# Optimization experiments

Measured on AMD Instinct MI355X. Metric: run time of the kernel, lower is better.

## Reference

```python
import jax, jax.numpy as jnp
import numpy as np

IN_F = 1024
OUT_F = 4096
SEARCH_SPACE = [1, 2, 4, 8, 16]  # block sizes; powers of 2 dividing both dims, capped at 16


def circ_avg(W, bs):
    """Project W [out,in] onto block-circulant structure with block size bs.

    Equivalent to trans_to_cir_meng: within each (bs x bs) block, average each
    wrap-around diagonal and rebuild a circulant block C[k, j] = c[(k - j) % bs].
    """
    q, p = W.shape[0] // bs, W.shape[1] // bs
    t = W.reshape(q, bs, p, bs).transpose(0, 2, 1, 3)  # [q, p, bs, bs]
    i = jnp.arange(bs)
    # rot[..., i, j] = t[..., i, (i + j) % bs]  (rotate rows so diagonals align in columns)
    rot = t[:, :, i[:, None], (i[:, None] + i[None, :]) % bs]  # [q, p, bs, bs]
    c = rot.mean(axis=2)  # [q, p, bs]  mean over each diagonal
    # circulant block: w[..., k, j] = c[..., (k - j) % bs]
    w = c[:, :, (i[:, None] - i[None, :]) % bs]  # [q, p, bs, bs]
    return w.transpose(0, 2, 1, 3).reshape(W.shape)


def setup_inputs() -> dict:
    key = jax.random.key(0)
    k1, k2, k3, k4 = jax.random.split(key, 4)
    x = jax.random.normal(k1, (16, 512, IN_F), dtype=jnp.float32)
    weight = jax.random.normal(k2, (OUT_F, IN_F), dtype=jnp.float32) * 0.02
    alphas = jax.random.normal(k3, (len(SEARCH_SPACE),), dtype=jnp.float32)
    bias = jax.random.normal(k4, (OUT_F,), dtype=jnp.float32) * 0.02
    return {"x": x, "weight": weight, "alphas": alphas, "bias": bias}


def reference(x, weight, alphas, bias):
    # soft NAS mixture over block sizes (tau=1, soft mode)
    a = jax.nn.softmax(alphas)
    W = a[0] * weight  # block_size 1 == original weight
    for idx, bs in enumerate(SEARCH_SPACE[1:], start=1):
        W = W + a[idx] * circ_avg(weight, bs)
    # F.linear: y = x @ W^T + b
    return jnp.einsum("bsi,oi->bso", x, W) + bias
```

## Files before the change

### kernel.cpp

```cpp
#include <hip/hip_runtime.h>

typedef __bf16 bf16;
typedef __bf16 bf16x8 __attribute__((ext_vector_type(8)));
typedef float floatx4 __attribute__((ext_vector_type(4)));

#define IN_F  1024
#define OUT_F 4096
#define M_DIM 8192
#define K_DIM 1024
#define N_DIM 4096

__device__ __forceinline__ unsigned short f2bf(float f) {
    unsigned int u = __float_as_uint(f);
    u += 0x7FFFu + ((u >> 16) & 1u);
    return (unsigned short)(u >> 16);
}

__global__ __launch_bounds__(256) void build_w_kernel(
    const float* __restrict__ W, const float* __restrict__ alphas,
    unsigned short* __restrict__ Wb)
{
    __shared__ __align__(16) float Wl[16 * 256];
    __shared__ __align__(16) float D2[2048];
    __shared__ float D4[1024];
    __shared__ float D8[512];
    __shared__ float D16[256];

    const int t = threadIdx.x;
    const int rb = blockIdx.x >> 2;
    const int cb = blockIdx.x & 3;
    const int row0 = rb * 16, col0 = cb * 256;

    const float4* src = (const float4*)(W + (size_t)row0 * IN_F + col0);
    #pragma unroll
    for (int j = 0; j < 4; ++j) {
        const int idx = j * 256 + t;
        const int r = idx >> 6, c4 = idx & 63;
        ((float4*)Wl)[r * 64 + c4] = src[(size_t)r * 256 + c4];
    }

    float av[5];
    float mx = -1e30f;
    #pragma unroll
    for (int j = 0; j < 5; ++j) { av[j] = alphas[j]; mx = fmaxf(mx, av[j]); }
    float s = 0.f;
    #pragma unroll
    for (int j = 0; j < 5; ++j) { av[j] = __expf(av[j] - mx); s += av[j]; }
    const float inv = 1.f / s;
    #pragma unroll
    for (int j = 0; j < 5; ++j) av[j] *= inv;
    #pragma unroll
    for (int e = 1; e <= 4; ++e) av[e] *= 1.0f / (float)(1 << e);

    __syncthreads();

    {
        const int c16 = t >> 4, d = t & 15;
        float acc = 0.f;
        #pragma unroll
        for (int r = 0; r < 16; ++r)
            acc += Wl[r * 256 + c16 * 16 + ((r + d) & 15)];
        D16[t] = acc;
    }
    #pragma unroll
    for (int it = 0; it < 2; ++it) {
        const int s8 = t + it * 256;
        const int d = s8 & 7, c8 = (s8 >> 3) & 31, r8 = s8 >> 8;
        float acc = 0.f;
        #pragma unroll
        for (int r = 0; r < 8; ++r)
            acc += Wl[(r8 * 8 + r) * 256 + c8 * 8 + ((r + d) & 7)];
        D8[s8] = acc;
    }
    #pragma unroll
    for (int it = 0; it < 4; ++it) {
        const int s4 = t + it * 256;
        const int d = s4 & 3, c4 = (s4 >> 2) & 63, r4 = s4 >> 8;
        float acc = 0.f;
        #pragma unroll
        for (int r = 0; r < 4; ++r)
            acc += Wl[(r4 * 4 + r) * 256 + c4 * 4 + ((r + d) & 3)];
        D4[s4] = acc;
    }
    #pragma unroll
    for (int it = 0; it < 8; ++it) {
        const int s2 = t + it * 256;
        const int d = s2 & 1, c2 = (s2 >> 1) & 127, r2 = s2 >> 8;
        D2[s2] = Wl[(r2 * 2) * 256 + c2 * 2 + d]
               + Wl[(r2 * 2 + 1) * 256 + c2 * 2 + ((1 + d) & 1)];
    }

    __syncthreads();

    const int k = t >> 4, jj = t & 15;
    float res[16];
    #pragma unroll
    for (int jb = 0; jb < 16; ++jb) {
        const int col = jb * 16 + jj;
        const int dd = k - col;
        res[jb] = av[0] * Wl[k * 256 + col]
                + av[1] * D2[((k >> 1) * 128 + (col >> 1)) * 2 + (dd & 1)]
                + av[2] * D4[((k >> 2) * 64  + (col >> 2)) * 4 + (dd & 3)]
                + av[3] * D8[((k >> 3) * 32  + (col >> 3)) * 8 + (dd & 7)]
                + av[4] * D16[(col >> 4) * 16 + (dd & 15)];
    }

    __syncthreads();
    unsigned short* st = (unsigned short*)D2;
    #pragma unroll
    for (int jb = 0; jb < 16; ++jb)
        st[k * 256 + jb * 16 + jj] = f2bf(res[jb]);
    __syncthreads();

    const uint4* p = (const uint4*)(st + k * 256 + jj * 16);
    uint4* dst = (uint4*)(Wb + (size_t)(row0 + k) * IN_F + col0 + jj * 16);
    dst[0] = p[0];
    dst[1] = p[1];
}

__global__ __launch_bounds__(256) void cvt_x_kernel(
    const float* __restrict__ x, uint4* __restrict__ xb)
{
    const int t = blockIdx.x * 256 + threadIdx.x;
    const float4* xv = (const float4*)x;
    const float4 v0 = xv[2 * t];
    const float4 v1 = xv[2 * t + 1];
    uint4 o;
    o.x = (unsigned)f2bf(v0.x) | ((unsigned)f2bf(v0.y) << 16);
    o.y = (unsigned)f2bf(v0.z) | ((unsigned)f2bf(v0.w) << 16);
    o.z = (unsigned)f2bf(v1.x) | ((unsigned)f2bf(v1.y) << 16);
    o.w = (unsigned)f2bf(v1.z) | ((unsigned)f2bf(v1.w) << 16);
    xb[t] = o;
}

__global__ __launch_bounds__(256) void gemm_bt_kernel(
    const bf16* __restrict__ A, const bf16* __restrict__ B,
    const float* __restrict__ bias, float* __restrict__ C)
{
    constexpr int N = N_DIM, K = K_DIM;
    constexpr int TM = 128, TN = 128, TK = 64;
    constexpr int NBLK = (M_DIM / TM) * (N_DIM / TN);

    __shared__ __align__(16) bf16 As[TM * TK];
    __shared__ __align__(16) bf16 Bs[TN * TK];

    const int t    = threadIdx.x;
    const int w    = t >> 6;
    const int l    = t & 63;
    const int quad = l >> 4;
    const int l16  = l & 15;
    const int x7   = l16 & 7;

    const int nb = N / TN;
    const int wgid = (blockIdx.x & 7) * (NBLK >> 3) + (blockIdx.x >> 3);
    const int bm = wgid / nb;
    const int bn = wgid % nb;

    const int wm = (w >> 1) * 64;
    const int wn = (w & 1) * 64;

    floatx4 acc[4][4] = {};

    int crow[4], ccol[4], loff[4];
    #pragma unroll
    for (int q = 0; q < 4; ++q) {
        const int chunk = q * 256 + t;
        crow[q] = chunk >> 3;
        ccol[q] = (((chunk & 7) ^ ((chunk >> 3) & 7)) * 8);
        loff[q] = (q * 256 + (t & ~63)) * 8;
    }

    const bf16* Abase = A + (size_t)bm * TM * K;
    const bf16* Bbase = B + (size_t)bn * TN * K;

    for (int kt = 0; kt < K; kt += TK) {
        #pragma unroll
        for (int q = 0; q < 4; ++q) {
            __builtin_amdgcn_global_load_lds(
                (const __attribute__((address_space(1))) void*)(Abase + (size_t)crow[q] * K + kt + ccol[q]),
                (__attribute__((address_space(3))) void*)(As + loff[q]), 16, 0, 0);
        }
        #pragma unroll
        for (int q = 0; q < 4; ++q) {
            __builtin_amdgcn_global_load_lds(
                (const __attribute__((address_space(1))) void*)(Bbase + (size_t)crow[q] * K + kt + ccol[q]),
                (__attribute__((address_space(3))) void*)(Bs + loff[q]), 16, 0, 0);
        }
        __syncthreads();

        #pragma unroll
        for (int ks = 0; ks < 2; ++ks) {
            bf16x8 af[4], bfr[4];
            const int kx = ((ks * 4 + quad) ^ x7) * 8;
            #pragma unroll
            for (int mt = 0; mt < 4; ++mt)
                af[mt] = *(const bf16x8*)(As + (wm + mt * 16 + l16) * TK + kx);
            #pragma unroll
            for (int nt = 0; nt < 4; ++nt)
                bfr[nt] = *(const bf16x8*)(Bs + (wn + nt * 16 + l16) * TK + kx);
            #pragma unroll
            for (int mt = 0; mt < 4; ++mt)
                #pragma unroll
                for (int nt = 0; nt < 4; ++nt)
                    acc[mt][nt] = __builtin_amdgcn_mfma_f32_16x16x32_bf16(
                        af[mt], bfr[nt], acc[mt][nt], 0, 0, 0);
        }
        __syncthreads();
    }

    float bv[4];
    #pragma unroll
    for (int nt = 0; nt < 4; ++nt)
        bv[nt] = bias[bn * TN + wn + nt * 16 + l16];

    float* Cbase = C + (size_t)(bm * TM + wm) * N + bn * TN + wn;
    #pragma unroll
    for (int mt = 0; mt < 4; ++mt) {
        #pragma unroll
        for (int r = 0; r < 4; ++r) {
            float* crowp = Cbase + (size_t)(mt * 16 + quad * 4 + r) * N;
            #pragma unroll
            for (int nt = 0; nt < 4; ++nt)
                crowp[nt * 16 + l16] = acc[mt][nt][r] + bv[nt];
        }
    }
}

extern "C" void kernel_launch(void* const* d_in, const int* in_sizes, int n_in,
                              void* d_out, int out_size, void* d_ws, size_t ws_size,
                              hipStream_t stream) {
    const float* x      = (const float*)d_in[0];
    const float* weight = (const float*)d_in[1];
    const float* alphas = (const float*)d_in[2];
    const float* bias   = (const float*)d_in[3];
    float* out = (float*)d_out;

    unsigned short* Wb = (unsigned short*)d_ws;
    unsigned short* Xb = (unsigned short*)((char*)d_ws + (size_t)OUT_F * IN_F * 2);

    build_w_kernel<<<(OUT_F / 16) * (IN_F / 256), 256, 0, stream>>>(weight, alphas, Wb);
    cvt_x_kernel<<<(M_DIM * K_DIM / 8) / 256, 256, 0, stream>>>(x, (uint4*)Xb);

    const int grid = (M_DIM / 128) * (N_DIM / 128);
    gemm_bt_kernel<<<grid, 256, 0, stream>>>((const bf16*)Xb, (const bf16*)Wb, bias, out);
}
```

Baseline: 248.4 us.

## Triple-buffer GEMM LDS staging with 256x128 tiles and 512-thread blocks

Result: faster. 237.6 us (-4.4%).

```diff
diff --git a/kernel.cpp b/kernel.cpp
--- a/kernel.cpp
+++ b/kernel.cpp
@@ -133,16 +133,21 @@
     xb[t] = o;
 }
 
-__global__ __launch_bounds__(256) void gemm_bt_kernel(
+#define TM 256
+#define TN 128
+#define TK 64
+#define A_SLOT_EL (TM * TK)
+#define B_SLOT_EL (TN * TK)
+#define SLOT_EL   (A_SLOT_EL + B_SLOT_EL)
+
+__global__ __launch_bounds__(512, 2) void gemm_bt_kernel(
     const bf16* __restrict__ A, const bf16* __restrict__ B,
     const float* __restrict__ bias, float* __restrict__ C)
 {
     constexpr int N = N_DIM, K = K_DIM;
-    constexpr int TM = 128, TN = 128, TK = 64;
-    constexpr int NBLK = (M_DIM / TM) * (N_DIM / TN);
-
-    __shared__ __align__(16) bf16 As[TM * TK];
-    __shared__ __align__(16) bf16 Bs[TN * TK];
+    constexpr int NT = K / TK;
+
+    __shared__ __align__(16) bf16 smem[3 * SLOT_EL];
 
     const int t    = threadIdx.x;
     const int w    = t >> 6;
@@ -152,9 +157,8 @@
     const int x7   = l16 & 7;
 
     const int nb = N / TN;
-    const int wgid = (blockIdx.x & 7) * (NBLK >> 3) + (blockIdx.x >> 3);
-    const int bm = wgid / nb;
-    const int bn = wgid % nb;
+    const int bm = blockIdx.x / nb;
+    const int bn = blockIdx.x % nb;
 
     const int wm = (w >> 1) * 64;
     const int wn = (w & 1) * 64;
@@ -164,49 +168,86 @@
     int crow[4], ccol[4], loff[4];
     #pragma unroll
     for (int q = 0; q < 4; ++q) {
-        const int chunk = q * 256 + t;
+        const int chunk = q * 512 + t;
         crow[q] = chunk >> 3;
-        ccol[q] = (((chunk & 7) ^ ((chunk >> 3) & 7)) * 8);
-        loff[q] = (q * 256 + (t & ~63)) * 8;
+        ccol[q] = ((chunk & 7) ^ ((chunk >> 3) & 7)) * 8;
+        loff[q] = (q * 512 + (t & ~63)) * 8;
     }
 
     const bf16* Abase = A + (size_t)bm * TM * K;
     const bf16* Bbase = B + (size_t)bn * TN * K;
 
-    for (int kt = 0; kt < K; kt += TK) {
-        #pragma unroll
-        for (int q = 0; q < 4; ++q) {
-            __builtin_amdgcn_global_load_lds(
-                (const __attribute__((address_space(1))) void*)(Abase + (size_t)crow[q] * K + kt + ccol[q]),
-                (__attribute__((address_space(3))) void*)(As + loff[q]), 16, 0, 0);
-        }
-        #pragma unroll
-        for (int q = 0; q < 4; ++q) {
-            __builtin_amdgcn_global_load_lds(
-                (const __attribute__((address_space(1))) void*)(Bbase + (size_t)crow[q] * K + kt + ccol[q]),
-                (__attribute__((address_space(3))) void*)(Bs + loff[q]), 16, 0, 0);
-        }
-        __syncthreads();
-
-        #pragma unroll
-        for (int ks = 0; ks < 2; ++ks) {
-            bf16x8 af[4], bfr[4];
-            const int kx = ((ks * 4 + quad) ^ x7) * 8;
-            #pragma unroll
-            for (int mt = 0; mt < 4; ++mt)
-                af[mt] = *(const bf16x8*)(As + (wm + mt * 16 + l16) * TK + kx);
-            #pragma unroll
-            for (int nt = 0; nt < 4; ++nt)
-                bfr[nt] = *(const bf16x8*)(Bs + (wn + nt * 16 + l16) * TK + kx);
-            #pragma unroll
-            for (int mt = 0; mt < 4; ++mt)
-                #pragma unroll
-                for (int nt = 0; nt < 4; ++nt)
-                    acc[mt][nt] = __builtin_amdgcn_mfma_f32_16x16x32_bf16(
-                        af[mt], bfr[nt], acc[mt][nt], 0, 0, 0);
-        }
-        __syncthreads();
-    }
+#define STAGE_A(KT, SLOT)                                                        \
+    do {                                                                         \
+        _Pragma("unroll")                                                        \
+        for (int q = 0; q < 4; ++q)                                              \
+            __builtin_amdgcn_global_load_lds(                                    \
+                (const __attribute__((address_space(1))) void*)(                 \
+                    Abase + (size_t)crow[q] * K + (KT) * TK + ccol[q]),          \
+                (__attribute__((address_space(3))) void*)((SLOT) + loff[q]),     \
+                16, 0, 0);                                                       \
+    } while (0)
+
+#define STAGE_B(KT, SLOT)                                                        \
+    do {                                                                         \
+        _Pragma("unroll")                                                        \
+        for (int q = 0; q < 2; ++q)                                              \
+            __builtin_amdgcn_global_load_lds(                                    \
+                (const __attribute__((address_space(1))) void*)(                 \
+                    Bbase + (size_t)crow[q] * K + (KT) * TK + ccol[q]),          \
+                (__attribute__((address_space(3))) void*)((SLOT) + A_SLOT_EL +   \
+                                                          loff[q]),              \
+                16, 0, 0);                                                       \
+    } while (0)
+
+#define PHASE(SA, SB, KS, STAGE_STMT)                                            \
+    do {                                                                         \
+        bf16x8 af[4], bfr[4];                                                    \
+        const int kx = (((KS) * 4 + quad) ^ x7) * 8;                             \
+        _Pragma("unroll")                                                        \
+        for (int mt = 0; mt < 4; ++mt)                                           \
+            af[mt] = *(const bf16x8*)((SA) + (wm + mt * 16 + l16) * TK + kx);    \
+        _Pragma("unroll")                                                        \
+        for (int nt = 0; nt < 4; ++nt)                                           \
+            bfr[nt] = *(const bf16x8*)((SB) + (wn + nt * 16 + l16) * TK + kx);   \
+        STAGE_STMT;                                                              \
+        __builtin_amdgcn_s_barrier();                                            \
+        __builtin_amdgcn_s_setprio(1);                                           \
+        _Pragma("unroll")                                                        \
+        for (int mt = 0; mt < 4; ++mt)                                           \
+            _Pragma("unroll")                                                    \
+            for (int nt = 0; nt < 4; ++nt)                                       \
+                acc[mt][nt] = __builtin_amdgcn_mfma_f32_16x16x32_bf16(           \
+                    af[mt], bfr[nt], acc[mt][nt], 0, 0, 0);                      \
+        __builtin_amdgcn_s_setprio(0);                                           \
+    } while (0)
+
+    bf16* s0 = smem;
+    bf16* s1 = smem + SLOT_EL;
+    bf16* s2 = smem + 2 * SLOT_EL;
+    STAGE_A(0, s0); STAGE_B(0, s0);
+    STAGE_A(1, s1); STAGE_B(1, s1);
+
+    #pragma unroll 1
+    for (int kt = 0; kt < NT; ++kt) {
+        if (kt == NT - 1)
+            asm volatile("s_waitcnt vmcnt(0)" ::: "memory");
+        else
+            asm volatile("s_waitcnt vmcnt(6)" ::: "memory");
+        __builtin_amdgcn_s_barrier();
+
+        bf16* Sa = s0;
+        bf16* Sb = s0 + A_SLOT_EL;
+        const bool st = (kt + 2 < NT);
+
+        PHASE(Sa, Sb, 0, if (st) STAGE_A(kt + 2, s2));
+        PHASE(Sa, Sb, 1, if (st) STAGE_B(kt + 2, s2));
+
+        bf16* tmp = s0; s0 = s1; s1 = s2; s2 = tmp;
+    }
+#undef PHASE
+#undef STAGE_A
+#undef STAGE_B
 
     float bv[4];
     #pragma unroll
@@ -241,6 +282,6 @@
     build_w_kernel<<<(OUT_F / 16) * (IN_F / 256), 256, 0, stream>>>(weight, alphas, Wb);
     cvt_x_kernel<<<(M_DIM * K_DIM / 8) / 256, 256, 0, stream>>>(x, (uint4*)Xb);
 
-    const int grid = (M_DIM / 128) * (N_DIM / 128);
-    gemm_bt_kernel<<<grid, 256, 0, stream>>>((const bf16*)Xb, (const bf16*)Wb, bias, out);
-}
+    const int grid = (M_DIM / TM) * (N_DIM / TN);
+    gemm_bt_kernel<<<grid, 512, 0, stream>>>((const bf16*)Xb, (const bf16*)Wb, bias, out);
+}
```

## Rewrite GEMM with 256x256 tiles and a 9-slot multi-stage async LDS pipeline

Applied to the files above, without the earlier changes.

Measured after the change: 233.2 us. -6.1%, faster.

```diff
diff --git a/kernel.cpp b/kernel.cpp
--- a/kernel.cpp
+++ b/kernel.cpp
@@ -133,95 +133,178 @@
     xb[t] = o;
 }
 
-__global__ __launch_bounds__(256) void gemm_bt_kernel(
+#define TM 256
+#define TN 256
+#define TK 64
+#define HALF_EL 8192
+#define NSLOT 9
+
+__global__ __launch_bounds__(512, 2) void gemm_bt_kernel(
     const bf16* __restrict__ A, const bf16* __restrict__ B,
     const float* __restrict__ bias, float* __restrict__ C)
 {
     constexpr int N = N_DIM, K = K_DIM;
-    constexpr int TM = 128, TN = 128, TK = 64;
-    constexpr int NBLK = (M_DIM / TM) * (N_DIM / TN);
-
-    __shared__ __align__(16) bf16 As[TM * TK];
-    __shared__ __align__(16) bf16 Bs[TN * TK];
+
+    __shared__ __align__(16) bf16 smem[NSLOT * HALF_EL];
 
     const int t    = threadIdx.x;
     const int w    = t >> 6;
     const int l    = t & 63;
     const int quad = l >> 4;
     const int l16  = l & 15;
-    const int x7   = l16 & 7;
+
+    const int wr = w >> 2;
+    const int wc = w & 3;
+    const int wm = wr * 128;
+    const int wn = wc * 64;
 
     const int nb = N / TN;
-    const int wgid = (blockIdx.x & 7) * (NBLK >> 3) + (blockIdx.x >> 3);
-    const int bm = wgid / nb;
-    const int bn = wgid % nb;
-
-    const int wm = (w >> 1) * 64;
-    const int wn = (w & 1) * 64;
-
-    floatx4 acc[4][4] = {};
-
-    int crow[4], ccol[4], loff[4];
-    #pragma unroll
-    for (int q = 0; q < 4; ++q) {
-        const int chunk = q * 256 + t;
-        crow[q] = chunk >> 3;
-        ccol[q] = (((chunk & 7) ^ ((chunk >> 3) & 7)) * 8);
-        loff[q] = (q * 256 + (t & ~63)) * 8;
-    }
-
-    const bf16* Abase = A + (size_t)bm * TM * K;
-    const bf16* Bbase = B + (size_t)bn * TN * K;
-
-    for (int kt = 0; kt < K; kt += TK) {
+    const int bm = blockIdx.x / nb;
+    const int bn = blockIdx.x % nb;
+
+    const int fko = l16 * 32 + ((quad ^ ((l16 >> 1) & 3)) * 8);
+
+    int sloff0, sloff1;
+    const bf16 *As0p, *As1p, *Bs0p, *Bs1p;
+    {
+        const int c0 = t, c1 = 512 + t;
+        const int r0 = c0 >> 2, r1 = c1 >> 2;
+        const int k0 = ((c0 & 3) ^ ((c0 >> 3) & 3)) * 8;
+        const int k1 = ((c1 & 3) ^ ((c1 >> 3) & 3)) * 8;
+        sloff0 = (t & ~63) * 8;
+        sloff1 = (512 + (t & ~63)) * 8;
+        const bf16* Abase = A + (size_t)bm * TM * K;
+        const bf16* Bbase = B + (size_t)bn * TN * K;
+        As0p = Abase + (size_t)r0 * K + k0;
+        As1p = Abase + (size_t)r1 * K + k1;
+        Bs0p = Bbase + (size_t)r0 * K + k0;
+        Bs1p = Bbase + (size_t)r1 * K + k1;
+    }
+
+    floatx4 acc[8][4] = {};
+
+#define GLL(SRC, DST)                                                         \
+    __builtin_amdgcn_global_load_lds(                                         \
+        (const __attribute__((address_space(1))) void*)(SRC),                 \
+        (__attribute__((address_space(3))) void*)(DST), 16, 0, 0)
+
+#define STAGE(TT, J, SL) do {                                                 \
+        const bf16* g0_ = ((J) & 1) ? Bs0p : As0p;                            \
+        const bf16* g1_ = ((J) & 1) ? Bs1p : As1p;                            \
+        const int ko_ = (TT) * TK + ((J) >> 1) * 32;                          \
+        bf16* lb_ = smem + (SL) * HALF_EL;                                    \
+        GLL(g0_ + ko_, lb_ + sloff0);                                         \
+        GLL(g1_ + ko_, lb_ + sloff1);                                         \
+    } while (0)
+
+#define MF(d, va, vb)                                                         \
+    d = __builtin_amdgcn_mfma_f32_16x16x32_bf16(va, vb, d, 0, 0, 0)
+
+    STAGE(0, 0, 0); STAGE(0, 1, 1); STAGE(0, 2, 2); STAGE(0, 3, 3);
+    STAGE(1, 0, 4); STAGE(1, 1, 5); STAGE(1, 2, 6);
+
+    bf16x8 af[8], bfr[4];
+    int s4 = 0;
+
+#define TILE_BODY(T, V0, V2, DO0, DO1, DO2, DO3) do {                         \
+    const int slA0 = s4;                                                      \
+    const int slB0 = s4 + 1 - ((s4 + 1 >= NSLOT) ? NSLOT : 0);                \
+    const int slA1 = s4 + 2 - ((s4 + 2 >= NSLOT) ? NSLOT : 0);                \
+    const int slB1 = s4 + 3 - ((s4 + 3 >= NSLOT) ? NSLOT : 0);                \
+    const int sp0  = s4 + 7 - ((s4 + 7 >= NSLOT) ? NSLOT : 0);                \
+    const int sp1  = s4 + 8 - ((s4 + 8 >= NSLOT) ? NSLOT : 0);                \
+                               \
+    asm volatile("s_waitcnt vmcnt(" V0 ")" ::: "memory");                     \
+    __builtin_amdgcn_s_barrier();                                             \
+    {                                                                         \
+        const bf16* a0_ = smem + slA0 * HALF_EL + wm * 32 + fko;              \
+        const bf16* b0_ = smem + slB0 * HALF_EL + wn * 32 + fko;              \
+        _Pragma("unroll")                                                     \
+        for (int m = 0; m < 8; ++m)                                           \
+            af[m] = *(const bf16x8*)(a0_ + m * 512);                          \
+        bfr[0] = *(const bf16x8*)(b0_);                                       \
+        bfr[1] = *(const bf16x8*)(b0_ + 512);                                 \
+        if (DO0) STAGE((T) + 1, 3, sp0);                                      \
+        __builtin_amdgcn_s_setprio(1);                                        \
+        _Pragma("unroll")                                                     \
+        for (int m = 0; m < 8; ++m) {                                         \
+            MF(acc[m][0], af[m], bfr[0]);                                     \
+            MF(acc[m][1], af[m], bfr[1]);                                     \
+        }                                                                     \
+        __builtin_amdgcn_s_setprio(0);                                        \
+                                     \
+        __builtin_amdgcn_s_barrier();                                         \
+        bfr[2] = *(const bf16x8*)(b0_ + 1024);                                \
+        bfr[3] = *(const bf16x8*)(b0_ + 1536);                                \
+        if (DO1) STAGE((T) + 2, 0, sp1);                                      \
+        __builtin_amdgcn_s_setprio(1);                                        \
+        _Pragma("unroll")                                                     \
+        for (int m = 0; m < 8; ++m) {                                         \
+            MF(acc[m][2], af[m], bfr[2]);                                     \
+            MF(acc[m][3], af[m], bfr[3]);                                     \
+        }                                                                     \
+        __builtin_amdgcn_s_setprio(0);                                        \
+    }                                                                         \
+                             \
+    asm volatile("s_waitcnt vmcnt(" V2 ")" ::: "memory");                     \
+    __builtin_amdgcn_s_barrier();                                             \
+    {                                                                         \
+        const bf16* a1_ = smem + slA1 * HALF_EL + wm * 32 + fko;              \
+        const bf16* b1_ = smem + slB1 * HALF_EL + wn * 32 + fko;              \
+        _Pragma("unroll")                                                     \
+        for (int m = 0; m < 8; ++m)                                           \
+            af[m] = *(const bf16x8*)(a1_ + m * 512);                          \
+        bfr[0] = *(const bf16x8*)(b1_);                                       \
+        bfr[1] = *(const bf16x8*)(b1_ + 512);                                 \
+        if (DO2) STAGE((T) + 2, 1, slA0);      \
+        __builtin_amdgcn_s_setprio(1);                                        \
+        _Pragma("unroll")                                                     \
+        for (int m = 0; m < 8; ++m) {                                         \
+            MF(acc[m][0], af[m], bfr[0]);                                     \
+            MF(acc[m][1], af[m], bfr[1]);                                     \
+        }                                                                     \
+        __builtin_amdgcn_s_setprio(0);                                        \
+                                                \
+        __builtin_amdgcn_s_barrier();                                         \
+        bfr[2] = *(const bf16x8*)(b1_ + 1024);                                \
+        bfr[3] = *(const bf16x8*)(b1_ + 1536);                                \
+        if (DO3) STAGE((T) + 2, 2, slB0);      \
+        __builtin_amdgcn_s_setprio(1);                                        \
+        _Pragma("unroll")                                                     \
+        for (int m = 0; m < 8; ++m) {                                         \
+            MF(acc[m][2], af[m], bfr[2]);                                     \
+            MF(acc[m][3], af[m], bfr[3]);                                     \
+        }                                                                     \
+        __builtin_amdgcn_s_setprio(0);                                        \
+    }                                                                         \
+    s4 += 4; if (s4 >= NSLOT) s4 -= NSLOT;                                    \
+} while (0)
+
+    #pragma unroll 1
+    for (int T = 0; T < 14; ++T)
+        TILE_BODY(T, "10", "10", true, true, true, true);
+    TILE_BODY(14, "10", "8", true, false, false, false);
+    TILE_BODY(15, "4",  "0", false, false, false, false);
+
+#undef TILE_BODY
+#undef STAGE
+#undef GLL
+#undef MF
+
+    float bv[4];
+    #pragma unroll
+    for (int nt = 0; nt < 4; ++nt)
+        bv[nt] = bias[bn * TN + wn + nt * 16 + l16];
+
+    float* Cbase = C + (size_t)(bm * TM + wm) * N + bn * TN + wn;
+    #pragma unroll
+    for (int m = 0; m < 8; ++m) {
         #pragma unroll
-        for (int q = 0; q < 4; ++q) {
-            __builtin_amdgcn_global_load_lds(
-                (const __attribute__((address_space(1))) void*)(Abase + (size_t)crow[q] * K + kt + ccol[q]),
-                (__attribute__((address_space(3))) void*)(As + loff[q]), 16, 0, 0);
-        }
-        #pragma unroll
-        for (int q = 0; q < 4; ++q) {
-            __builtin_amdgcn_global_load_lds(
-                (const __attribute__((address_space(1))) void*)(Bbase + (size_t)crow[q] * K + kt + ccol[q]),
-                (__attribute__((address_space(3))) void*)(Bs + loff[q]), 16, 0, 0);
-        }
-        __syncthreads();
-
-        #pragma unroll
-        for (int ks = 0; ks < 2; ++ks) {
-            bf16x8 af[4], bfr[4];
-            const int kx = ((ks * 4 + quad) ^ x7) * 8;
-            #pragma unroll
-            for (int mt = 0; mt < 4; ++mt)
-                af[mt] = *(const bf16x8*)(As + (wm + mt * 16 + l16) * TK + kx);
+        for (int r = 0; r < 4; ++r) {
+            float* crowp = Cbase + (size_t)(m * 16 + quad * 4 + r) * N;
             #pragma unroll
             for (int nt = 0; nt < 4; ++nt)
-                bfr[nt] = *(const bf16x8*)(Bs + (wn + nt * 16 + l16) * TK + kx);
-            #pragma unroll
-            for (int mt = 0; mt < 4; ++mt)
-                #pragma unroll
-                for (int nt = 0; nt < 4; ++nt)
-                    acc[mt][nt] = __builtin_amdgcn_mfma_f32_16x16x32_bf16(
-                        af[mt], bfr[nt], acc[mt][nt], 0, 0, 0);
-        }
-        __syncthreads();
-    }
-
-    float bv[4];
-    #pragma unroll
-    for (int nt = 0; nt < 4; ++nt)
-        bv[nt] = bias[bn * TN + wn + nt * 16 + l16];
-
-    float* Cbase = C + (size_t)(bm * TM + wm) * N + bn * TN + wn;
-    #pragma unroll
-    for (int mt = 0; mt < 4; ++mt) {
-        #pragma unroll
-        for (int r = 0; r < 4; ++r) {
-            float* crowp = Cbase + (size_t)(mt * 16 + quad * 4 + r) * N;
-            #pragma unroll
-            for (int nt = 0; nt < 4; ++nt)
-                crowp[nt * 16 + l16] = acc[mt][nt][r] + bv[nt];
+                crowp[nt * 16 + l16] = acc[m][nt][r] + bv[nt];
         }
     }
 }
@@ -241,6 +324,6 @@
     build_w_kernel<<<(OUT_F / 16) * (IN_F / 256), 256, 0, stream>>>(weight, alphas, Wb);
     cvt_x_kernel<<<(M_DIM * K_DIM / 8) / 256, 256, 0, stream>>>(x, (uint4*)Xb);
 
-    const int grid = (M_DIM / 128) * (N_DIM / 128);
-    gemm_bt_kernel<<<grid, 256, 0, stream>>>((const bf16*)Xb, (const bf16*)Wb, bias, out);
-}
+    const int grid = (M_DIM / TM) * (N_DIM / TN);
+    gemm_bt_kernel<<<grid, 512, 0, stream>>>((const bf16*)Xb, (const bf16*)Wb, bias, out);
+}
```
